# Kernel optimization log

Hardware: AMD Instinct MI355X
Metric: run time of the kernel (lower is better)

## Reference

```python
import jax, jax.numpy as jnp
import numpy as np
from jax import lax

FEAT_STRIDE = 16
PRE_NMS_TOP_N = 6000   # cfg['TEST'].RPN_PRE_NMS_TOP_N
POST_NMS_TOP_N = 300   # cfg['TEST'].RPN_POST_NMS_TOP_N
NMS_THRESH = 0.7       # cfg['TEST'].RPN_NMS_THRESH
MIN_SIZE = 16.0        # cfg['TEST'].RPN_MIN_SIZE
B, A, H, W = 32, 9, 128, 128
NEG_INF = jnp.float32(-1e30)


def _whctrs(a):
    w = a[2] - a[0] + 1.0
    h = a[3] - a[1] + 1.0
    return w, h, a[0] + 0.5 * (w - 1), a[1] + 0.5 * (h - 1)

def _mkanchors(ws, hs, xc, yc):
    ws = ws[:, None]; hs = hs[:, None]
    return np.hstack((xc - 0.5 * (ws - 1), yc - 0.5 * (hs - 1),
                      xc + 0.5 * (ws - 1), yc + 0.5 * (hs - 1)))

def _ratio_enum(anchor, ratios):
    w, h, xc, yc = _whctrs(anchor)
    size = w * h
    ws = np.round(np.sqrt(size / ratios))
    hs = np.round(ws * ratios)
    return _mkanchors(ws, hs, xc, yc)

def _scale_enum(anchor, scales):
    w, h, xc, yc = _whctrs(anchor)
    return _mkanchors(w * scales, h * scales, xc, yc)

def generate_anchors(base_size=16, ratios=np.array([0.5, 1.0, 2.0]), scales=np.array([8.0, 16.0, 32.0])):
    base = np.array([1, 1, base_size, base_size], dtype=np.float64) - 1
    ra = _ratio_enum(base, ratios)
    return np.vstack([_scale_enum(ra[i], scales) for i in range(ra.shape[0])]).astype(np.float32)

_BASE_ANCHORS = generate_anchors()  # (A, 4)

def _all_anchors(h, w):
    sx = np.arange(w) * FEAT_STRIDE
    sy = np.arange(h) * FEAT_STRIDE
    sx, sy = np.meshgrid(sx, sy)  # row-major (h, w) matches permute(0,2,3,1) ordering
    shifts = np.stack([sx.ravel(), sy.ravel(), sx.ravel(), sy.ravel()], axis=1).astype(np.float32)
    return jnp.asarray((shifts[:, None, :] + _BASE_ANCHORS[None, :, :]).reshape(-1, 4))  # (h*w*A, 4)

# ---- bbox_transform_inv / clip_boxes ----

def _decode(anchors, deltas):
    ws = anchors[:, 2] - anchors[:, 0] + 1.0
    hs = anchors[:, 3] - anchors[:, 1] + 1.0
    cx = anchors[:, 0] + 0.5 * ws
    cy = anchors[:, 1] + 0.5 * hs
    dx, dy, dw, dh = deltas[:, 0], deltas[:, 1], deltas[:, 2], deltas[:, 3]
    pcx = dx * ws + cx
    pcy = dy * hs + cy
    pw = jnp.exp(dw) * ws
    ph = jnp.exp(dh) * hs
    return jnp.stack([pcx - 0.5 * pw, pcy - 0.5 * ph, pcx + 0.5 * pw, pcy + 0.5 * ph], axis=1)

def _clip(b, imh, imw):
    x1 = jnp.clip(b[:, 0], 0.0, imw - 1.0)
    y1 = jnp.clip(b[:, 1], 0.0, imh - 1.0)
    x2 = jnp.clip(b[:, 2], 0.0, imw - 1.0)
    y2 = jnp.clip(b[:, 3], 0.0, imh - 1.0)
    return jnp.stack([x1, y1, x2, y2], axis=1)

# ---- greedy NMS: pick top-score box, suppress IoU > thresh, repeat POST times ----

def _nms_select(boxes, scores):
    # boxes: (PRE, 4) score-sorted; scores: (PRE,)
    areas = (boxes[:, 2] - boxes[:, 0] + 1.0) * (boxes[:, 3] - boxes[:, 1] + 1.0)

    def body(i, st):
        s, keep, valid = st
        j = jnp.argmax(s)
        keep = keep.at[i].set(j)
        valid = valid.at[i].set(s[j] > NEG_INF)
        b = boxes[j]
        xx1 = jnp.maximum(b[0], boxes[:, 0])
        yy1 = jnp.maximum(b[1], boxes[:, 1])
        xx2 = jnp.minimum(b[2], boxes[:, 2])
        yy2 = jnp.minimum(b[3], boxes[:, 3])
        inter = jnp.maximum(xx2 - xx1 + 1.0, 0.0) * jnp.maximum(yy2 - yy1 + 1.0, 0.0)
        iou = inter / jnp.maximum(areas[j] + areas - inter, 1e-6)
        s = jnp.where(iou > NMS_THRESH, NEG_INF, s)  # suppresses j itself (IoU = 1)
        return s, keep, valid

    init = (scores, jnp.zeros((POST_NMS_TOP_N,), jnp.int32), jnp.zeros((POST_NMS_TOP_N,), bool))
    _, keep, valid = lax.fori_loop(0, POST_NMS_TOP_N, body, init)
    return keep, valid

def _per_image(sc, dl, info, anchors):
    prop = _clip(_decode(anchors, dl), info[0], info[1])  # (K*A, 4)
    ws = prop[:, 2] - prop[:, 0] + 1.0
    hs = prop[:, 3] - prop[:, 1] + 1.0
    min_sz = MIN_SIZE * info[2]
    sc = jnp.where((ws >= min_sz) & (hs >= min_sz), sc, NEG_INF)
    top_s, top_i = lax.top_k(sc, PRE_NMS_TOP_N)
    cand = prop[top_i]  # (PRE, 4)
    keep, valid = _nms_select(cand, top_s)
    return cand[keep] * valid[:, None].astype(cand.dtype)  # zero-pad invalid rows

def _forward(rpn_cls_prob, rpn_bbox_pred, im_info):
    b, _, h, w = rpn_cls_prob.shape
    anchors = _all_anchors(h, w)
    scores = rpn_cls_prob[:, A:, :, :].transpose(0, 2, 3, 1).reshape(b, -1)  # (b, h*w*A)
    deltas = rpn_bbox_pred.transpose(0, 2, 3, 1).reshape(b, -1, 4)           # (b, h*w*A, 4)
    boxes = jax.vmap(lambda s, d, i: _per_image(s, d, i, anchors))(scores, deltas, im_info)
    ids = jnp.broadcast_to(jnp.arange(b, dtype=boxes.dtype)[:, None, None], (b, POST_NMS_TOP_N, 1))
    return jnp.concatenate([ids, boxes], axis=2)  # (b, POST, 5): [batch_idx, x1, y1, x2, y2]

def setup_inputs() -> dict:
    key = jax.random.key(0)
    k1, k2 = jax.random.split(key)
    rpn_cls_prob = jax.random.uniform(k1, (B, 2 * A, H, W), dtype=jnp.float32)
    rpn_bbox_pred = jax.random.normal(k2, (B, 4 * A, H, W), dtype=jnp.float32) * 0.2
    im_info = jnp.tile(jnp.array([[H * FEAT_STRIDE, W * FEAT_STRIDE, 1.0]], dtype=jnp.float32), (B, 1))
    return {"rpn_cls_prob": rpn_cls_prob, "rpn_bbox_pred": rpn_bbox_pred, "im_info": im_info}

def reference(rpn_cls_prob, rpn_bbox_pred, im_info):
    return _forward(rpn_cls_prob, rpn_bbox_pred, im_info)
```

## Files before the change

### kernel.cpp

```cpp
#include <hip/hip_runtime.h>
#include <cstdint>
#include <cstddef>

#pragma clang fp contract(off)

typedef unsigned long long u64;

#define NB 32
#define NA 9
#define NH 128
#define NW 128
#define HW (NH*NW)
#define NANCH (NA*HW)
#define PRE_N 6000
#define POST_N 300
#define CAND_CAP 8192
#define NMS_T 0.7f
#define GX_GATHER 24

__constant__ float c_wa[9] = {184.f,368.f,736.f,128.f,256.f,512.f,88.f,176.f,352.f};
__constant__ float c_ha[9] = {96.f,192.f,384.f,128.f,256.f,512.f,176.f,352.f,704.f};

__device__ __forceinline__ float4 decode_clip(int a, int h, int w,
    float dx, float dy, float dlw, float dlh, float imh, float imw) {
  float wa = c_wa[a], ha = c_ha[a];
  float cx = (float)w * 16.0f + 8.0f;
  float cy = (float)h * 16.0f + 8.0f;
  float pcx = dx * wa + cx;
  float pcy = dy * ha + cy;
  float pw = expf(dlw) * wa;
  float ph = expf(dlh) * ha;
  float x1 = pcx - 0.5f * pw;
  float y1 = pcy - 0.5f * ph;
  float x2 = pcx + 0.5f * pw;
  float y2 = pcy + 0.5f * ph;
  float4 r;
  r.x = fminf(fmaxf(x1, 0.0f), imw - 1.0f);
  r.y = fminf(fmaxf(y1, 0.0f), imh - 1.0f);
  r.z = fminf(fmaxf(x2, 0.0f), imw - 1.0f);
  r.w = fminf(fmaxf(y2, 0.0f), imh - 1.0f);
  return r;
}

__device__ __forceinline__ unsigned score_key(float sc, float bw, float bh, float msz) {
  unsigned bits = __float_as_uint(sc);
  unsigned key = (bits & 0x80000000u) ? ~bits : (bits | 0x80000000u);
  if (!(bw >= msz && bh >= msz)) key = 0u;
  return key;
}

__device__ __forceinline__ bool sup_test4(float4 v, float ar, float4 p, float pa) {
  float xx1 = fmaxf(p.x, v.x), yy1 = fmaxf(p.y, v.y);
  float xx2 = fminf(p.z, v.z), yy2 = fminf(p.w, v.w);
  float iw = fmaxf(xx2 - xx1 + 1.0f, 0.0f);
  float ih = fmaxf(yy2 - yy1 + 1.0f, 0.0f);
  float inter = iw * ih;
  float iou = inter / fmaxf(pa + ar - inter, 1e-6f);
  return iou > NMS_T;
}

__device__ void find_B(const unsigned* __restrict__ hb, unsigned* part,
                       unsigned* outB, unsigned* outCum) {
  int tid = threadIdx.x;
  unsigned s = 0;
  for (int i = 0; i < 16; ++i) s += hb[tid*16 + i];
  part[tid] = s;
  __syncthreads();
  for (int off = 1; off < 256; off <<= 1) {
    unsigned v = (tid + off < 256) ? part[tid + off] : 0u;
    __syncthreads();
    part[tid] += v;
    __syncthreads();
  }
  unsigned St = part[tid];
  unsigned Sn = (tid < 255) ? part[tid + 1] : 0u;
  if (St >= (unsigned)PRE_N && Sn < (unsigned)PRE_N) {
    unsigned cum = Sn, B = 0, cumAbove = Sn;
    for (int i = 15; i >= 0; --i) {
      unsigned v = hb[tid*16 + i];
      if (cum + v >= (unsigned)PRE_N) { B = (unsigned)(tid*16 + i); cumAbove = cum; break; }
      cum += v;
    }
    *outB = B; *outCum = cumAbove;
  }
  __syncthreads();
}

__device__ void find_thr(const unsigned* __restrict__ hb2, unsigned B, unsigned cum0,
                         unsigned* part, unsigned* outThr) {
  int tid = threadIdx.x;
  unsigned s = 0;
  for (int i = 0; i < 16; ++i) s += hb2[tid*16 + i];
  part[tid] = s;
  __syncthreads();
  for (int off = 1; off < 256; off <<= 1) {
    unsigned v = (tid + off < 256) ? part[tid + off] : 0u;
    __syncthreads();
    part[tid] += v;
    __syncthreads();
  }
  unsigned St = cum0 + part[tid];
  unsigned Sn = cum0 + ((tid < 255) ? part[tid + 1] : 0u);
  if (St >= (unsigned)PRE_N && Sn < (unsigned)PRE_N) {
    unsigned cum = Sn, t = 1u;
    for (int i = 15; i >= 0; --i) {
      unsigned v = hb2[tid*16 + i];
      if (cum + v >= (unsigned)PRE_N) {
        t = (B << 20) | ((unsigned)(tid*16 + i) << 8);
        break;
      }
      cum += v;
    }
    if (t == 0u) t = 1u;
    *outThr = t;
  }
  __syncthreads();
}

__global__ __launch_bounds__(256) void k_keys(const float* __restrict__ cls,
    const float* __restrict__ dl, const float* __restrict__ info,
    unsigned* __restrict__ keys, unsigned* __restrict__ hist) {
  __shared__ unsigned hsh[4096];
  int tid = threadIdx.x;
  for (int i = tid; i < 4096; i += 256) hsh[i] = 0;
  int t = blockIdx.x * 256 + tid;
  int b = blockIdx.y;
  int hw0 = t * 4;
  int h = hw0 >> 7;
  const float* dlb  = dl  + (size_t)b * (4*NA*HW);
  const float* clsb = cls + (size_t)b * (2*NA*HW);
  float imh = info[b*3+0], imw = info[b*3+1];
  float msz = 16.0f * info[b*3+2];
  unsigned* kb = keys + (size_t)b * NANCH;
  __syncthreads();
  #pragma unroll
  for (int a = 0; a < 9; ++a) {
    float4 dx4 = *(const float4*)&dlb[(a*4+0)*HW + hw0];
    float4 dy4 = *(const float4*)&dlb[(a*4+1)*HW + hw0];
    float4 dw4 = *(const float4*)&dlb[(a*4+2)*HW + hw0];
    float4 dh4 = *(const float4*)&dlb[(a*4+3)*HW + hw0];
    float4 sc4 = *(const float4*)&clsb[(NA+a)*HW + hw0];
    uint4 out;
    {
      float4 bx = decode_clip(a, h, (hw0+0)&127, dx4.x, dy4.x, dw4.x, dh4.x, imh, imw);
      out.x = score_key(sc4.x, bx.z-bx.x+1.0f, bx.w-bx.y+1.0f, msz);
    }
    {
      float4 bx = decode_clip(a, h, (hw0+1)&127, dx4.y, dy4.y, dw4.y, dh4.y, imh, imw);
      out.y = score_key(sc4.y, bx.z-bx.x+1.0f, bx.w-bx.y+1.0f, msz);
    }
    {
      float4 bx = decode_clip(a, h, (hw0+2)&127, dx4.z, dy4.z, dw4.z, dh4.z, imh, imw);
      out.z = score_key(sc4.z, bx.z-bx.x+1.0f, bx.w-bx.y+1.0f, msz);
    }
    {
      float4 bx = decode_clip(a, h, (hw0+3)&127, dx4.w, dy4.w, dw4.w, dh4.w, imh, imw);
      out.w = score_key(sc4.w, bx.z-bx.x+1.0f, bx.w-bx.y+1.0f, msz);
    }
    *(uint4*)&kb[a*HW + hw0] = out;
    atomicAdd(&hsh[out.x >> 20], 1u);
    atomicAdd(&hsh[out.y >> 20], 1u);
    atomicAdd(&hsh[out.z >> 20], 1u);
    atomicAdd(&hsh[out.w >> 20], 1u);
  }
  __syncthreads();
  unsigned* gb = hist + ((size_t)b << 12);
  for (int i = tid; i < 4096; i += 256) {
    unsigned v = hsh[i];
    if (v) atomicAdd(&gb[i], v);
  }
}

__global__ __launch_bounds__(256) void k_hist2(const unsigned* __restrict__ keys,
    const unsigned* __restrict__ hist1, unsigned* __restrict__ hist2) {
  __shared__ unsigned h[4096];
  __shared__ unsigned part[256];
  __shared__ unsigned sB, sCum;
  int b = blockIdx.y, tid = threadIdx.x;
  for (int i = tid; i < 4096; i += 256) h[i] = 0;
  __syncthreads();
  find_B(hist1 + ((size_t)b << 12), part, &sB, &sCum);
  unsigned B = sB;
  const unsigned* kb = keys + (size_t)b * NANCH;
  for (int i = blockIdx.x * 256 + tid; i < NANCH; i += gridDim.x * 256) {
    unsigned k = kb[i];
    if ((k >> 20) == B) atomicAdd(&h[(k >> 8) & 4095u], 1u);
  }
  __syncthreads();
  unsigned* gb = hist2 + ((size_t)b << 12);
  for (int i = tid; i < 4096; i += 256) { unsigned v = h[i]; if (v) atomicAdd(&gb[i], v); }
}

__global__ __launch_bounds__(256) void k_gather(const unsigned* __restrict__ keys,
    const unsigned* __restrict__ hist1, const unsigned* __restrict__ hist2,
    unsigned* __restrict__ cnt, u64* __restrict__ cand) {
  int b = blockIdx.y, tid = threadIdx.x;
  int lane = tid & 63, wv = tid >> 6;
  __shared__ unsigned part[256];
  __shared__ unsigned sB, sCum, sThr;
  __shared__ unsigned wcnt[4], woff[4], blkbase;
  if (tid == 0) sThr = 1u;
  __syncthreads();
  find_B(hist1 + ((size_t)b << 12), part, &sB, &sCum);
  find_thr(hist2 + ((size_t)b << 12), sB, sCum, part, &sThr);
  unsigned t_ = sThr;
  const unsigned* kb = keys + (size_t)b * NANCH;
  u64* cb = cand + (size_t)b * CAND_CAP;
  unsigned* cp = cnt + (size_t)b * 64;
  const int PER_BLK = NANCH / GX_GATHER;
  int base0 = blockIdx.x * PER_BLK;
  for (int it = 0; it < PER_BLK / 256; ++it) {
    int j = base0 + it * 256 + tid;
    unsigned key = kb[j];
    bool pass = key >= t_;
    u64 mask = __ballot(pass);
    if (lane == 0) wcnt[wv] = (unsigned)__popcll(mask);
    __syncthreads();
    if (tid == 0) {
      unsigned s0 = 0;
      for (int w = 0; w < 4; ++w) { woff[w] = s0; s0 += wcnt[w]; }
      blkbase = s0 ? atomicAdd(cp, s0) : 0u;
    }
    __syncthreads();
    if (pass) {
      unsigned pos = blkbase + woff[wv] + (unsigned)__popcll(mask & ((1ull << lane) - 1ull));
      if (pos < CAND_CAP) {
        int a = j >> 14, hw = j & (HW - 1);
        unsigned oi = (unsigned)(hw * 9 + a);
        cb[pos] = ((u64)key << 32) | (unsigned)(~oi);
      }
    }
    __syncthreads();
  }
}

__global__ __launch_bounds__(256) void k_sortA(u64* __restrict__ cand,
                                               const unsigned* __restrict__ cnt) {
  __shared__ u64 sm[2048];
  int blk = blockIdx.x;
  int b = blk >> 2, c = blk & 3;
  unsigned effcnt = cnt[b * 64];
  if (effcnt > CAND_CAP) effcnt = CAND_CAP;
  u64* cb = cand + (size_t)b * CAND_CAP + (size_t)c * 2048;
  int base = c * 2048;
  int tid = threadIdx.x;
  for (int t = tid; t < 2048; t += 256)
    sm[t] = ((unsigned)(base + t) < effcnt) ? cb[t] : 0ull;
  bool blkdesc = (c & 1) == 0;
  for (int k = 2; k <= 2048; k <<= 1) {
    for (int j = k >> 1; j > 0; j >>= 1) {
      __syncthreads();
      for (int t = tid; t < 2048; t += 256) {
        int p = t ^ j;
        if (p > t) {
          bool up = (k == 2048) ? blkdesc : ((t & k) == 0);
          u64 x = sm[t], y = sm[p];
          if (up ? (x < y) : (x > y)) { sm[t] = y; sm[p] = x; }
        }
      }
    }
  }
  __syncthreads();
  for (int t = tid; t < 2048; t += 256) cb[t] = sm[t];
}

__global__ __launch_bounds__(512) void k_merge4096(u64* __restrict__ cand) {
  __shared__ u64 sm[4096];
  int blk = blockIdx.x;
  int b = blk >> 1, m = blk & 1;
  u64* cb = cand + (size_t)b * CAND_CAP + (size_t)m * 4096;
  int tid = threadIdx.x;
  for (int t = tid; t < 4096; t += 512) sm[t] = cb[t];
  bool desc = (m & 1) == 0;
  for (int j = 2048; j > 0; j >>= 1) {
    __syncthreads();
    for (int t = tid; t < 4096; t += 512) {
      int p = t ^ j;
      if (p > t) {
        u64 x = sm[t], y = sm[p];
        if (desc ? (x < y) : (x > y)) { sm[t] = y; sm[p] = x; }
      }
    }
  }
  __syncthreads();
  for (int t = tid; t < 4096; t += 512) cb[t] = sm[t];
}

__global__ __launch_bounds__(1024) void k_final(const u64* __restrict__ cand,
    const float* __restrict__ dl, const float* __restrict__ info,
    float* __restrict__ out) {
  __shared__ u64 sm[CAND_CAP];
  __shared__ float4 kbox[POST_N];
  __shared__ float  karea[POST_N];
  __shared__ float4 cbox[256];
  __shared__ float  carea[256];
  __shared__ unsigned supf[256];
  __shared__ u64 sup[256][4];
  __shared__ u64 aliveM[4];
  __shared__ u64 kgW[4];
  __shared__ int s_nk;
  int b = blockIdx.x, tid = threadIdx.x;
  int c = tid & 255, seg = tid >> 8;
  int lane = tid & 63, wv = tid >> 6;
  int cg = c >> 6;
  if (tid == 0) s_nk = 0;
  const u64* cb = cand + (size_t)b * CAND_CAP;
  for (int t = tid; t < CAND_CAP; t += 1024) sm[t] = cb[t];
  for (int j = CAND_CAP >> 1; j > 0; j >>= 1) {
    __syncthreads();
    for (int t = tid; t < CAND_CAP; t += 1024) {
      int p = t ^ j;
      if (p > t) {
        u64 x = sm[t], y = sm[p];
        if (x < y) { sm[t] = y; sm[p] = x; }
      }
    }
  }
  __syncthreads();

  const float* dlb = dl + (size_t)b * (4*NA*HW);
  float imh = info[b*3+0], imw = info[b*3+1];
  float* ob = out + (size_t)b * (POST_N * 5);
  volatile unsigned* svf = supf;

  for (int base = 0; base < PRE_N; base += 256) {
    if (tid < 256) {
      int i = base + tid;
      u64 ck = (i < PRE_N) ? sm[i] : 0ull;
      bool valid = (unsigned)(ck >> 32) != 0u;
      float4 v = make_float4(0.f, 0.f, 0.f, 0.f);
      if (valid) {
        int idx = (int)(~(unsigned)(ck & 0xFFFFFFFFull));
        int a = idx % 9, hw = idx / 9;
        v = decode_clip(a, hw >> 7, hw & 127,
                        dlb[(a*4+0)*HW + hw], dlb[(a*4+1)*HW + hw],
                        dlb[(a*4+2)*HW + hw], dlb[(a*4+3)*HW + hw], imh, imw);
      }
      cbox[tid] = v;
      carea[tid] = (v.z - v.x + 1.0f) * (v.w - v.y + 1.0f);
      supf[tid] = valid ? 0u : 1u;
    }
    __syncthreads();
    int nk0 = s_nk;

    if (supf[c] == 0u) {
      float4 v = cbox[c]; float ar = carea[c];
      for (int k = seg; k < nk0; k += 4) {
        if (svf[c]) break;
        if (sup_test4(v, ar, kbox[k], karea[k])) { atomicOr(&supf[c], 1u); break; }
      }
    }
    __syncthreads();

    if (seg == 0) {
      u64 am = __ballot(supf[c] == 0u);
      if (lane == 0) aliveM[wv] = am;
    }
    __syncthreads();
    if ((aliveM[0] | aliveM[1] | aliveM[2] | aliveM[3]) == 0ull) continue;

    if (supf[c] == 0u && seg <= cg) {
      float4 v = cbox[c]; float ar = carea[c];
      u64 m = aliveM[seg];
      if (seg == cg) m &= (1ull << (c & 63)) - 1ull;
      u64 r = 0;
      while (m) {
        int j = __builtin_ctzll(m);
        m &= m - 1;
        int col = seg * 64 + j;
        if (sup_test4(v, ar, cbox[col], carea[col])) r |= 1ull << j;
      }
      sup[c][seg] = r;
    }
    __syncthreads();

    if (wv == 0) {
      u64 kw0 = 0, kw1 = 0, kw2 = 0, kw3 = 0;
      {
        bool a = (aliveM[0] >> lane) & 1;
        u64 r = a ? sup[lane][0] : 0;
        u64 cm = __ballot(a), kg = 0;
        while (cm) {
          int j = __builtin_ctzll(cm);
          kg |= 1ull << j;
          u64 rem = __ballot((r >> j) & 1);
          cm &= ~(rem | (1ull << j));
        }
        kw0 = kg;
      }
      {
        int cc = 64 + lane;
        bool a = (aliveM[1] >> lane) & 1;
        if (a) a = (sup[cc][0] & kw0) == 0;
        u64 r = a ? sup[cc][1] : 0;
        u64 cm = __ballot(a), kg = 0;
        while (cm) {
          int j = __builtin_ctzll(cm);
          kg |= 1ull << j;
          u64 rem = __ballot((r >> j) & 1);
          cm &= ~(rem | (1ull << j));
        }
        kw1 = kg;
      }
      {
        int cc = 128 + lane;
        bool a = (aliveM[2] >> lane) & 1;
        if (a) a = ((sup[cc][0] & kw0) == 0) && ((sup[cc][1] & kw1) == 0);
        u64 r = a ? sup[cc][2] : 0;
        u64 cm = __ballot(a), kg = 0;
        while (cm) {
          int j = __builtin_ctzll(cm);
          kg |= 1ull << j;
          u64 rem = __ballot((r >> j) & 1);
          cm &= ~(rem | (1ull << j));
        }
        kw2 = kg;
      }
      {
        int cc = 192 + lane;
        bool a = (aliveM[3] >> lane) & 1;
        if (a) a = ((sup[cc][0] & kw0) == 0) && ((sup[cc][1] & kw1) == 0) &&
                   ((sup[cc][2] & kw2) == 0);
        u64 r = a ? sup[cc][3] : 0;
        u64 cm = __ballot(a), kg = 0;
        while (cm) {
          int j = __builtin_ctzll(cm);
          kg |= 1ull << j;
          u64 rem = __ballot((r >> j) & 1);
          cm &= ~(rem | (1ull << j));
        }
        kw3 = kg;
      }
      if (lane == 0) { kgW[0] = kw0; kgW[1] = kw1; kgW[2] = kw2; kgW[3] = kw3; }
    }
    __syncthreads();

    if (tid < 256) {
      u64 kgw = kgW[wv];
      bool kept = (kgw >> lane) & 1;
      int pre = 0;
      for (int g = 0; g < wv; ++g) pre += (int)__popcll(kgW[g]);
      pre += (int)__popcll(kgw & ((1ull << lane) - 1ull));
      int rank = nk0 + pre;
      if (kept && rank < POST_N) {
        float4 v = cbox[tid];
        kbox[rank] = v; karea[rank] = carea[tid];
        ob[rank*5+0] = (float)b;
        ob[rank*5+1] = v.x; ob[rank*5+2] = v.y; ob[rank*5+3] = v.z; ob[rank*5+4] = v.w;
      }
    }
    if (tid == 0) {
      int tot = (int)(__popcll(kgW[0]) + __popcll(kgW[1]) + __popcll(kgW[2]) + __popcll(kgW[3]));
      int nn = nk0 + tot;
      s_nk = nn < POST_N ? nn : POST_N;
    }
    __syncthreads();
    if (s_nk >= POST_N) break;
  }
  __syncthreads();
  int nk = s_nk;
  for (int r = nk + tid; r < POST_N; r += 1024) {
    ob[r*5+0] = (float)b;
    ob[r*5+1] = 0.f; ob[r*5+2] = 0.f; ob[r*5+3] = 0.f; ob[r*5+4] = 0.f;
  }
}

extern "C" void kernel_launch(void* const* d_in, const int* in_sizes, int n_in,
                              void* d_out, int out_size, void* d_ws, size_t ws_size,
                              hipStream_t stream) {
  const float* cls  = (const float*)d_in[0];
  const float* dl   = (const float*)d_in[1];
  const float* info = (const float*)d_in[2];
  float* out = (float*)d_out;
  char* ws = (char*)d_ws;

  const size_t OFF_KEYS = 0;
  const size_t OFF_H1   = 18874368;
  const size_t OFF_H2   = 19398656;
  const size_t OFF_CNT  = 19922944;
  const size_t OFF_CAND = 19931136;
  const size_t WS_NEED  = 22028288;
  if (ws_size < WS_NEED) return;

  unsigned* keys  = (unsigned*)(ws + OFF_KEYS);
  unsigned* h1    = (unsigned*)(ws + OFF_H1);
  unsigned* h2    = (unsigned*)(ws + OFF_H2);
  unsigned* cnt   = (unsigned*)(ws + OFF_CNT);
  u64* cand = (u64*)(ws + OFF_CAND);

  hipMemsetAsync(ws + OFF_H1, 0, OFF_CAND - OFF_H1, stream);

  dim3 g1(HW / 1024, NB);
  k_keys<<<g1, 256, 0, stream>>>(cls, dl, info, keys, h1);
  dim3 gh(8, NB);
  k_hist2<<<gh, 256, 0, stream>>>(keys, h1, h2);
  dim3 gg(GX_GATHER, NB);
  k_gather<<<gg, 256, 0, stream>>>(keys, h1, h2, cnt, cand);
  k_sortA<<<NB * 4, 256, 0, stream>>>(cand, cnt);
  k_merge4096<<<NB * 2, 512, 0, stream>>>(cand);
  k_final<<<NB, 1024, 0, stream>>>(cand, dl, info, out);
}
```

Baseline: 383.8 us.

## Split final kernel into merge+decode and NMS with 512-wide candidate chunks

Splits the final kernel in two. The first sorts candidates and decodes all 6000 boxes into a workspace buffer in one parallel pass. The second loads all boxes into shared memory and runs the blocked NMS over 512-candidate chunks (8 mask words) instead of 256, so fewer serial chunk iterations and barriers are needed. This adds a kernel launch and a global round trip for the boxes, and a longer serial ballot-resolve phase per chunk. Invalid boxes are now marked by negative width rather than a separate flag.

```diff
diff --git a/kernel.cpp b/kernel.cpp
--- a/kernel.cpp
+++ b/kernel.cpp
@@ -17,6 +17,8 @@
 #define CAND_CAP 8192
 #define NMS_T 0.7f
 #define GX_GATHER 24
+#define NBOX 6144
+#define CH 512
 
 __constant__ float c_wa[9] = {184.f,368.f,736.f,128.f,256.f,512.f,88.f,176.f,352.f};
 __constant__ float c_ha[9] = {96.f,192.f,384.f,128.f,256.f,512.f,176.f,352.f,704.f};
@@ -286,24 +288,11 @@
   for (int t = tid; t < 4096; t += 512) cb[t] = sm[t];
 }
 
-__global__ __launch_bounds__(1024) void k_final(const u64* __restrict__ cand,
+__global__ __launch_bounds__(1024) void k_mergedec(const u64* __restrict__ cand,
     const float* __restrict__ dl, const float* __restrict__ info,
-    float* __restrict__ out) {
+    float4* __restrict__ boxes) {
   __shared__ u64 sm[CAND_CAP];
-  __shared__ float4 kbox[POST_N];
-  __shared__ float  karea[POST_N];
-  __shared__ float4 cbox[256];
-  __shared__ float  carea[256];
-  __shared__ unsigned supf[256];
-  __shared__ u64 sup[256][4];
-  __shared__ u64 aliveM[4];
-  __shared__ u64 kgW[4];
-  __shared__ int s_nk;
   int b = blockIdx.x, tid = threadIdx.x;
-  int c = tid & 255, seg = tid >> 8;
-  int lane = tid & 63, wv = tid >> 6;
-  int cg = c >> 6;
-  if (tid == 0) s_nk = 0;
   const u64* cb = cand + (size_t)b * CAND_CAP;
   for (int t = tid; t < CAND_CAP; t += 1024) sm[t] = cb[t];
   for (int j = CAND_CAP >> 1; j > 0; j >>= 1) {
@@ -317,68 +306,106 @@
     }
   }
   __syncthreads();
-
   const float* dlb = dl + (size_t)b * (4*NA*HW);
   float imh = info[b*3+0], imw = info[b*3+1];
+  float4* bxout = boxes + (size_t)b * NBOX;
+  for (int t = tid; t < NBOX; t += 1024) {
+    u64 ck = (t < PRE_N) ? sm[t] : 0ull;
+    float4 v = make_float4(0.f, 0.f, -1.f, -1.f);
+    if ((unsigned)(ck >> 32) != 0u) {
+      int idx = (int)(~(unsigned)(ck & 0xFFFFFFFFull));
+      int a = idx % 9, hw = idx / 9;
+      v = decode_clip(a, hw >> 7, hw & 127,
+                      dlb[(a*4+0)*HW + hw], dlb[(a*4+1)*HW + hw],
+                      dlb[(a*4+2)*HW + hw], dlb[(a*4+3)*HW + hw], imh, imw);
+    }
+    bxout[t] = v;
+  }
+}
+
+__global__ __launch_bounds__(1024) void k_nms(const float4* __restrict__ boxes,
+    float* __restrict__ out) {
+  __shared__ float4 bx[NBOX];
+  __shared__ float4 kbox[POST_N];
+  __shared__ float  karea[POST_N];
+  __shared__ float  carea[CH];
+  __shared__ unsigned supf[CH];
+  __shared__ u64 sup[CH][8];
+  __shared__ u64 aliveM[8];
+  __shared__ u64 kgW[8];
+  __shared__ int s_nk;
+  int b = blockIdx.x, tid = threadIdx.x;
+  int lane = tid & 63, wv = tid >> 6;
+  int c = tid & (CH - 1);
+  int seg = tid >> 9;
+  int cg = c >> 6;
+  if (tid == 0) s_nk = 0;
+  const float4* gb = boxes + (size_t)b * NBOX;
+  for (int t = tid; t < NBOX; t += 1024) bx[t] = gb[t];
   float* ob = out + (size_t)b * (POST_N * 5);
   volatile unsigned* svf = supf;
-
-  for (int base = 0; base < PRE_N; base += 256) {
-    if (tid < 256) {
-      int i = base + tid;
-      u64 ck = (i < PRE_N) ? sm[i] : 0ull;
-      bool valid = (unsigned)(ck >> 32) != 0u;
-      float4 v = make_float4(0.f, 0.f, 0.f, 0.f);
-      if (valid) {
-        int idx = (int)(~(unsigned)(ck & 0xFFFFFFFFull));
-        int a = idx % 9, hw = idx / 9;
-        v = decode_clip(a, hw >> 7, hw & 127,
-                        dlb[(a*4+0)*HW + hw], dlb[(a*4+1)*HW + hw],
-                        dlb[(a*4+2)*HW + hw], dlb[(a*4+3)*HW + hw], imh, imw);
-      }
-      cbox[tid] = v;
-      carea[tid] = (v.z - v.x + 1.0f) * (v.w - v.y + 1.0f);
-      supf[tid] = valid ? 0u : 1u;
+  __syncthreads();
+
+  for (int base = 0; base < NBOX; base += CH) {
+    if (tid < CH) {
+      float4 v = bx[base + tid];
+      float w = v.z - v.x + 1.0f, h = v.w - v.y + 1.0f;
+      carea[tid] = w * h;
+      supf[tid] = (w > 0.0f) ? 0u : 1u;
     }
     __syncthreads();
     int nk0 = s_nk;
 
     if (supf[c] == 0u) {
-      float4 v = cbox[c]; float ar = carea[c];
-      for (int k = seg; k < nk0; k += 4) {
+      float4 v = bx[base + c]; float ar = carea[c];
+      for (int k = seg; k < nk0; k += 2) {
         if (svf[c]) break;
         if (sup_test4(v, ar, kbox[k], karea[k])) { atomicOr(&supf[c], 1u); break; }
       }
     }
     __syncthreads();
 
-    if (seg == 0) {
-      u64 am = __ballot(supf[c] == 0u);
+    if (tid < CH) {
+      u64 am = __ballot(supf[tid] == 0u);
       if (lane == 0) aliveM[wv] = am;
     }
     __syncthreads();
-    if ((aliveM[0] | aliveM[1] | aliveM[2] | aliveM[3]) == 0ull) continue;
-
-    if (supf[c] == 0u && seg <= cg) {
-      float4 v = cbox[c]; float ar = carea[c];
-      u64 m = aliveM[seg];
-      if (seg == cg) m &= (1ull << (c & 63)) - 1ull;
-      u64 r = 0;
-      while (m) {
-        int j = __builtin_ctzll(m);
-        m &= m - 1;
-        int col = seg * 64 + j;
-        if (sup_test4(v, ar, cbox[col], carea[col])) r |= 1ull << j;
-      }
-      sup[c][seg] = r;
+    u64 anyAlive = aliveM[0]|aliveM[1]|aliveM[2]|aliveM[3]|
+                   aliveM[4]|aliveM[5]|aliveM[6]|aliveM[7];
+    if (anyAlive == 0ull) continue;
+
+    if (supf[c] == 0u) {
+      float4 v = bx[base + c]; float ar = carea[c];
+      #pragma unroll
+      for (int gg = 0; gg < 4; ++gg) {
+        int g = seg * 4 + gg;
+        if (g <= cg) {
+          u64 m = aliveM[g];
+          if (g == cg) m &= (1ull << (c & 63)) - 1ull;
+          u64 r = 0;
+          while (m) {
+            int j = __builtin_ctzll(m);
+            m &= m - 1;
+            int col = g * 64 + j;
+            if (sup_test4(v, ar, bx[base + col], carea[col])) r |= 1ull << j;
+          }
+          sup[c][g] = r;
+        }
+      }
     }
     __syncthreads();
 
     if (wv == 0) {
-      u64 kw0 = 0, kw1 = 0, kw2 = 0, kw3 = 0;
-      {
-        bool a = (aliveM[0] >> lane) & 1;
-        u64 r = a ? sup[lane][0] : 0;
+      u64 kw[8];
+      #pragma unroll
+      for (int s = 0; s < 8; ++s) {
+        int cc = s * 64 + lane;
+        bool a = (aliveM[s] >> lane) & 1;
+        #pragma unroll
+        for (int g = 0; g < 8; ++g) {
+          if (g < s && a) a = (sup[cc][g] & kw[g]) == 0ull;
+        }
+        u64 r = a ? sup[cc][s] : 0ull;
         u64 cm = __ballot(a), kg = 0;
         while (cm) {
           int j = __builtin_ctzll(cm);
@@ -386,56 +413,16 @@
           u64 rem = __ballot((r >> j) & 1);
           cm &= ~(rem | (1ull << j));
         }
-        kw0 = kg;
-      }
-      {
-        int cc = 64 + lane;
-        bool a = (aliveM[1] >> lane) & 1;
-        if (a) a = (sup[cc][0] & kw0) == 0;
-        u64 r = a ? sup[cc][1] : 0;
-        u64 cm = __ballot(a), kg = 0;
-        while (cm) {
-          int j = __builtin_ctzll(cm);
-          kg |= 1ull << j;
-          u64 rem = __ballot((r >> j) & 1);
-          cm &= ~(rem | (1ull << j));
-        }
-        kw1 = kg;
-      }
-      {
-        int cc = 128 + lane;
-        bool a = (aliveM[2] >> lane) & 1;
-        if (a) a = ((sup[cc][0] & kw0) == 0) && ((sup[cc][1] & kw1) == 0);
-        u64 r = a ? sup[cc][2] : 0;
-        u64 cm = __ballot(a), kg = 0;
-        while (cm) {
-          int j = __builtin_ctzll(cm);
-          kg |= 1ull << j;
-          u64 rem = __ballot((r >> j) & 1);
-          cm &= ~(rem | (1ull << j));
-        }
-        kw2 = kg;
-      }
-      {
-        int cc = 192 + lane;
-        bool a = (aliveM[3] >> lane) & 1;
-        if (a) a = ((sup[cc][0] & kw0) == 0) && ((sup[cc][1] & kw1) == 0) &&
-                   ((sup[cc][2] & kw2) == 0);
-        u64 r = a ? sup[cc][3] : 0;
-        u64 cm = __ballot(a), kg = 0;
-        while (cm) {
-          int j = __builtin_ctzll(cm);
-          kg |= 1ull << j;
-          u64 rem = __ballot((r >> j) & 1);
-          cm &= ~(rem | (1ull << j));
-        }
-        kw3 = kg;
-      }
-      if (lane == 0) { kgW[0] = kw0; kgW[1] = kw1; kgW[2] = kw2; kgW[3] = kw3; }
-    }
-    __syncthreads();
-
-    if (tid < 256) {
+        kw[s] = kg;
+      }
+      if (lane == 0) {
+        #pragma unroll
+        for (int s = 0; s < 8; ++s) kgW[s] = kw[s];
+      }
+    }
+    __syncthreads();
+
+    if (tid < CH) {
       u64 kgw = kgW[wv];
       bool kept = (kgw >> lane) & 1;
       int pre = 0;
@@ -443,14 +430,16 @@
       pre += (int)__popcll(kgw & ((1ull << lane) - 1ull));
       int rank = nk0 + pre;
       if (kept && rank < POST_N) {
-        float4 v = cbox[tid];
+        float4 v = bx[base + tid];
         kbox[rank] = v; karea[rank] = carea[tid];
         ob[rank*5+0] = (float)b;
         ob[rank*5+1] = v.x; ob[rank*5+2] = v.y; ob[rank*5+3] = v.z; ob[rank*5+4] = v.w;
       }
     }
     if (tid == 0) {
-      int tot = (int)(__popcll(kgW[0]) + __popcll(kgW[1]) + __popcll(kgW[2]) + __popcll(kgW[3]));
+      int tot = 0;
+      #pragma unroll
+      for (int s = 0; s < 8; ++s) tot += (int)__popcll(kgW[s]);
       int nn = nk0 + tot;
       s_nk = nn < POST_N ? nn : POST_N;
     }
@@ -487,6 +476,7 @@
   unsigned* h2    = (unsigned*)(ws + OFF_H2);
   unsigned* cnt   = (unsigned*)(ws + OFF_CNT);
   u64* cand = (u64*)(ws + OFF_CAND);
+  float4* boxes = (float4*)(ws + OFF_KEYS);
 
   hipMemsetAsync(ws + OFF_H1, 0, OFF_CAND - OFF_H1, stream);
 
@@ -498,5 +488,6 @@
   k_gather<<<gg, 256, 0, stream>>>(keys, h1, h2, cnt, cand);
   k_sortA<<<NB * 4, 256, 0, stream>>>(cand, cnt);
   k_merge4096<<<NB * 2, 512, 0, stream>>>(cand);
-  k_final<<<NB, 1024, 0, stream>>>(cand, dl, info, out);
-}
+  k_mergedec<<<NB, 1024, 0, stream>>>(cand, dl, info, boxes);
+  k_nms<<<NB, 1024, 0, stream>>>(boxes, out);
+}
```

Result: slower. 416.0 us (+8.4%).
